# Kernel tuning notes

Measured on AMD Instinct MI355X. Metric: run time of the kernel, lower is better.

The kernel has to match this reference:

```python
import jax, jax.numpy as jnp
import numpy as np

N_NODES = 50000
N_EDGES = 800000
EMBED = 128
HEADS = 8
HEAD_DIM = EMBED // HEADS  # 16
HIDDEN = 512
EPS = 1e-5
SLOPE = 0.2  # DGL GATConv default negative_slope


def setup_inputs() -> dict:
    key = jax.random.key(0)
    ks = jax.random.split(key, 16)
    s = 0.05
    return {
        "x": jax.random.normal(ks[0], (N_NODES, EMBED), dtype=jnp.float32),
        "src": jax.random.randint(ks[1], (N_EDGES,), 0, N_NODES),
        "dst": jax.random.randint(ks[2], (N_EDGES,), 0, N_NODES),
        # GATConv params: fc weight stored as [in, out] (i.e. torch weight transposed)
        "W": jax.random.normal(ks[3], (EMBED, HEADS * HEAD_DIM), dtype=jnp.float32) * s,
        "attn_l": jax.random.normal(ks[4], (HEADS, HEAD_DIM), dtype=jnp.float32) * s,
        "attn_r": jax.random.normal(ks[5], (HEADS, HEAD_DIM), dtype=jnp.float32) * s,
        "gat_bias": jnp.zeros((EMBED,), dtype=jnp.float32),
        # BatchNorm1d affine params (training-mode batch stats used in math)
        "gamma1": jnp.ones((EMBED,), dtype=jnp.float32),
        "beta1": jnp.zeros((EMBED,), dtype=jnp.float32),
        "gamma2": jnp.ones((EMBED,), dtype=jnp.float32),
        "beta2": jnp.zeros((EMBED,), dtype=jnp.float32),
        # FFN weights stored as [in, out]
        "W1": jax.random.normal(ks[6], (EMBED, HIDDEN), dtype=jnp.float32) * s,
        "b1": jnp.zeros((HIDDEN,), dtype=jnp.float32),
        "W2": jax.random.normal(ks[7], (HIDDEN, EMBED), dtype=jnp.float32) * s,
        "b2": jnp.zeros((EMBED,), dtype=jnp.float32),
    }


def _batchnorm(y, gamma, beta):
    mu = jnp.mean(y, axis=0)
    var = jnp.var(y, axis=0)  # biased variance, as torch BN uses for normalization
    return gamma * (y - mu) * jax.lax.rsqrt(var + EPS) + beta


def reference(x, src, dst, W, attn_l, attn_r, gat_bias,
              gamma1, beta1, gamma2, beta2, W1, b1, W2, b2):
    N = x.shape[0]
    # ---- GATConv ----
    feat = (x @ W).reshape(N, HEADS, HEAD_DIM)              # [N,H,D]
    el = jnp.sum(feat * attn_l, axis=-1)                    # [N,H]
    er = jnp.sum(feat * attn_r, axis=-1)                    # [N,H]
    e = jax.nn.leaky_relu(el[src] + er[dst], SLOPE)         # [E,H]
    # segment softmax over incoming edges of each dst node
    m = jax.ops.segment_max(e, dst, num_segments=N)         # [N,H] (-inf for empty)
    ex = jnp.exp(e - m[dst])                                # [E,H]
    denom = jax.ops.segment_sum(ex, dst, num_segments=N)    # [N,H]
    a = ex / denom[dst]                                     # [E,H]
    msg = feat[src] * a[:, :, None]                         # [E,H,D]
    rst = jax.ops.segment_sum(msg, dst, num_segments=N)     # [N,H,D]
    rst = rst + gat_bias.reshape(HEADS, HEAD_DIM)
    h = x + rst.reshape(N, EMBED)                           # skip connection
    # ---- FFN block: BN -> skip(MLP) -> BN ----
    h = _batchnorm(h, gamma1, beta1)
    y = jax.nn.relu(h @ W1 + b1) @ W2 + b2
    h = _batchnorm(h + y, gamma2, beta2)
    return h
```

## Files before the change

### kernel.cpp

```cpp
#include <hip/hip_runtime.h>

#define NCH 128
#define NH  8
#define HID 512
#define SLOPE 0.2f
#define BN_EPS 1e-5f
#define LDP 136
#define NPW 4

typedef __attribute__((ext_vector_type(8))) short short8;
typedef __attribute__((ext_vector_type(4))) float floatx4;

__device__ inline unsigned short f2bf(float f) {
  unsigned u = __float_as_uint(f);
  u += 0x7fffu + ((u >> 16) & 1u);
  return (unsigned short)(u >> 16);
}
__device__ inline float bflo(unsigned u) { return __uint_as_float(u << 16); }
__device__ inline float bfhi(unsigned u) { return __uint_as_float(u & 0xffff0000u); }

__global__ void prep_all(const float* __restrict__ W, unsigned short* __restrict__ WT,
                         const float* __restrict__ W1, unsigned short* __restrict__ w1f,
                         const float* __restrict__ W2, unsigned short* __restrict__ w2f,
                         float* __restrict__ stats, int* __restrict__ cnt, int N) {
  int b = blockIdx.x, tid = threadIdx.x;
  if (b < 64) {
    int i = b * 256 + tid;
    int n = i >> 7, k = i & 127;
    WT[i] = f2bf(W[k * NCH + n]);
  } else if (b < 320) {
    int i = (b - 64) * 256 + tid;
    int ntile = i >> 11, kk = (i >> 9) & 3, lane = (i >> 3) & 63, j = i & 7;
    int k = kk * 32 + (lane >> 4) * 8 + j;
    int n = ntile * 16 + (lane & 15);
    w1f[i] = f2bf(W1[k * HID + n]);
  } else if (b < 576) {
    int i = (b - 320) * 256 + tid;
    int ch = i >> 14, nt = (i >> 11) & 7, kk = (i >> 9) & 3, lane = (i >> 3) & 63, j = i & 7;
    int k = ch * 128 + kk * 32 + (lane >> 4) * 8 + j;
    int n = nt * 16 + (lane & 15);
    w2f[i] = f2bf(W2[k * NCH + n]);
  } else if (b < 596) {
    int i = (b - 576) * 256 + tid;
    ((float4*)stats)[i] = make_float4(0.f, 0.f, 0.f, 0.f);
  } else {
    int i = (b - 596) * 256 + tid;
    int n4 = (N + 3) >> 2;
    if (i < n4) ((int4*)cnt)[i] = make_int4(0, 0, 0, 0);
  }
}

__global__ __launch_bounds__(256) void feat_hist(const float* __restrict__ x,
                                                 const unsigned short* __restrict__ WT,
                                                 const float* __restrict__ attn_l,
                                                 const float* __restrict__ attn_r,
                                                 unsigned short* __restrict__ featb,
                                                 float* __restrict__ el, float* __restrict__ er,
                                                 int N,
                                                 const int* __restrict__ dst, int* __restrict__ cnt,
                                                 int E, int FB) {
  __shared__ unsigned short rowX[64 * LDP];
  __shared__ unsigned short wt[128 * LDP];
  __shared__ float alr[256];
  if (blockIdx.x >= FB) {
    int i = (blockIdx.x - FB) * 256 + threadIdx.x;
    if (i < E) atomicAdd(&cnt[dst[i]], 1);
    return;
  }
  int tid = threadIdx.x;
  int r0 = blockIdx.x * 64;
  int lane = tid & 63, wid = tid >> 6;
  int quad = lane >> 4, lc = lane & 15;
  int mrow = (wid & 1) * 32;
  int chalf = (wid >> 1) * 64;

  alr[tid] = (tid < 128) ? attn_l[tid] : attn_r[tid - 128];
  {
    int n = tid >> 1, kg = (tid & 1) * 64;
    const uint4* g = (const uint4*)(WT + n * NCH + kg);
    uint4* l = (uint4*)&wt[n * LDP + kg];
    for (int i = 0; i < 8; i++) l[i] = g[i];
  }
  {
    int r = tid >> 2, kg = (tid & 3) * 32;
    int gr = r0 + r;
    unsigned short tmp[32];
    if (gr < N) {
      const float4* gp = (const float4*)(x + (size_t)gr * NCH + kg);
      for (int i = 0; i < 8; i++) {
        float4 v = gp[i];
        tmp[i * 4 + 0] = f2bf(v.x); tmp[i * 4 + 1] = f2bf(v.y);
        tmp[i * 4 + 2] = f2bf(v.z); tmp[i * 4 + 3] = f2bf(v.w);
      }
    } else {
      for (int i = 0; i < 32; i++) tmp[i] = 0;
    }
    uint4* l = (uint4*)&rowX[r * LDP + kg];
    const uint4* s = (const uint4*)tmp;
    for (int i = 0; i < 4; i++) l[i] = s[i];
  }
  __syncthreads();

  floatx4 acc[2][4];
  for (int rt = 0; rt < 2; rt++) for (int tt = 0; tt < 4; tt++) acc[rt][tt] = (floatx4)(0.f);
  for (int kk = 0; kk < 4; kk++) {
    short8 a0 = *(const short8*)&rowX[(mrow + lc) * LDP + kk * 32 + quad * 8];
    short8 a1 = *(const short8*)&rowX[(mrow + 16 + lc) * LDP + kk * 32 + quad * 8];
    for (int tt = 0; tt < 4; tt++) {
      short8 b = *(const short8*)&wt[(chalf + tt * 16 + lc) * LDP + kk * 32 + quad * 8];
      acc[0][tt] = __builtin_amdgcn_mfma_f32_16x16x32_bf16(a0, b, acc[0][tt], 0, 0, 0);
      acc[1][tt] = __builtin_amdgcn_mfma_f32_16x16x32_bf16(a1, b, acc[1][tt], 0, 0, 0);
    }
  }
  __syncthreads();
  for (int rt = 0; rt < 2; rt++)
    for (int tt = 0; tt < 4; tt++)
      for (int r = 0; r < 4; r++)
        rowX[(mrow + rt * 16 + quad * 4 + r) * LDP + chalf + tt * 16 + lc] = f2bf(acc[rt][tt][r]);
  __syncthreads();
  {
    int r = tid >> 2, kg = (tid & 3) * 32;
    int gr = r0 + r;
    if (gr < N) {
      uint4* gp = (uint4*)(featb + (size_t)gr * NCH + kg);
      const uint4* l = (const uint4*)&rowX[r * LDP + kg];
      for (int i = 0; i < 4; i++) gp[i] = l[i];
    }
  }
  for (int p = tid; p < 512; p += 256) {
    int row = p >> 3, h = p & 7;
    int gr = r0 + row;
    if (gr < N) {
      const unsigned* rp = (const unsigned*)&rowX[row * LDP + h * 16];
      float sl = 0.f, sr = 0.f;
      for (int q = 0; q < 8; q++) {
        unsigned u = rp[q];
        float lo = bflo(u), hi = bfhi(u);
        int c = h * 16 + 2 * q;
        sl += lo * alr[c] + hi * alr[c + 1];
        sr += lo * alr[128 + c] + hi * alr[128 + c + 1];
      }
      el[gr * NH + h] = sl;
      er[gr * NH + h] = sr;
    }
  }
}

__global__ void scan_part(const int* __restrict__ cnt, int* __restrict__ off,
                          int* __restrict__ bsum, int N) {
  __shared__ int sh[256];
  int t = threadIdx.x, i = blockIdx.x * 256 + t;
  int v = (i < N) ? cnt[i] : 0;
  sh[t] = v; __syncthreads();
  for (int d = 1; d < 256; d <<= 1) {
    int u = (t >= d) ? sh[t - d] : 0;
    __syncthreads();
    sh[t] += u;
    __syncthreads();
  }
  if (i < N) off[i] = sh[t] - v;
  if (t == 255) bsum[blockIdx.x] = sh[255];
}

__global__ void scan_add2(int* __restrict__ off, const int* __restrict__ bsum,
                          int* __restrict__ cursor, int N, int nb) {
  __shared__ int sh[256];
  int t = threadIdx.x;
  int v = (t < nb) ? bsum[t] : 0;
  sh[t] = v; __syncthreads();
  for (int d = 1; d < 256; d <<= 1) {
    int u = (t >= d) ? sh[t - d] : 0;
    __syncthreads();
    sh[t] += u;
    __syncthreads();
  }
  int pref = (blockIdx.x > 0) ? sh[blockIdx.x - 1] : 0;
  int i = blockIdx.x * 256 + t;
  if (i < N) {
    int w = off[i] + pref;
    off[i] = w;
    cursor[i] = w;
  }
}

__global__ void edge_scatter(const int* __restrict__ src, const int* __restrict__ dst,
                             int* __restrict__ cursor, int* __restrict__ ssrc, int E) {
  int i = blockIdx.x * 256 + threadIdx.x;
  if (i < E) {
    int p = atomicAdd(&cursor[dst[i]], 1);
    ssrc[p] = src[i];
  }
}

__global__ __launch_bounds__(256) void gat_gather6(const int* __restrict__ ssrc,
                                                   const int* __restrict__ off,
                                                   const int* __restrict__ cnt,
                                                   const float* __restrict__ el,
                                                   const float* __restrict__ er,
                                                   const unsigned short* __restrict__ featb,
                                                   const float* __restrict__ x,
                                                   const float* __restrict__ gatb,
                                                   float* __restrict__ hbuf,
                                                   float* __restrict__ stats, int N) {
  __shared__ float ps[4][128], pq[4][128];
  int tid = threadIdx.x;
  int lane = tid & 63, w = tid >> 6;
  int hme = lane >> 3;
  int c0 = 2 * lane;
  float gb0 = gatb[c0], gb1 = gatb[c0 + 1];
  float s0 = 0.f, s1 = 0.f, q0 = 0.f, q1 = 0.f;
  int base = blockIdx.x * (4 * NPW) + w * NPW;
  for (int j = 0; j < NPW; j++) {
    int node = base + j;
    if (node >= N) break;
    node = __builtin_amdgcn_readfirstlane(node);
    float erh = er[node * NH + hme];
    int beg = __builtin_amdgcn_readfirstlane(off[node]);
    int num = __builtin_amdgcn_readfirstlane(cnt[node]);
    const int* sp = ssrc + beg;
    float acc0 = 0.f, acc1 = 0.f, den = 0.f;
    int i = 0;
    for (; i + 8 <= num; i += 8) {
      int n0 = __builtin_amdgcn_readfirstlane(sp[i + 0]);
      int n1 = __builtin_amdgcn_readfirstlane(sp[i + 1]);
      int n2 = __builtin_amdgcn_readfirstlane(sp[i + 2]);
      int n3 = __builtin_amdgcn_readfirstlane(sp[i + 3]);
      int n4 = __builtin_amdgcn_readfirstlane(sp[i + 4]);
      int n5 = __builtin_amdgcn_readfirstlane(sp[i + 5]);
      int n6 = __builtin_amdgcn_readfirstlane(sp[i + 6]);
      int n7 = __builtin_amdgcn_readfirstlane(sp[i + 7]);
      unsigned f0 = ((const unsigned*)(featb + (size_t)n0 * NCH))[lane];
      unsigned f1 = ((const unsigned*)(featb + (size_t)n1 * NCH))[lane];
      unsigned f2 = ((const unsigned*)(featb + (size_t)n2 * NCH))[lane];
      unsigned f3 = ((const unsigned*)(featb + (size_t)n3 * NCH))[lane];
      unsigned f4 = ((const unsigned*)(featb + (size_t)n4 * NCH))[lane];
      unsigned f5 = ((const unsigned*)(featb + (size_t)n5 * NCH))[lane];
      unsigned f6 = ((const unsigned*)(featb + (size_t)n6 * NCH))[lane];
      unsigned f7 = ((const unsigned*)(featb + (size_t)n7 * NCH))[lane];
      float e0 = el[n0 * NH + hme] + erh, e1 = el[n1 * NH + hme] + erh;
      float e2 = el[n2 * NH + hme] + erh, e3 = el[n3 * NH + hme] + erh;
      float e4 = el[n4 * NH + hme] + erh, e5 = el[n5 * NH + hme] + erh;
      float e6 = el[n6 * NH + hme] + erh, e7 = el[n7 * NH + hme] + erh;
      e0 = e0 > 0.f ? e0 : SLOPE * e0;  e1 = e1 > 0.f ? e1 : SLOPE * e1;
      e2 = e2 > 0.f ? e2 : SLOPE * e2;  e3 = e3 > 0.f ? e3 : SLOPE * e3;
      e4 = e4 > 0.f ? e4 : SLOPE * e4;  e5 = e5 > 0.f ? e5 : SLOPE * e5;
      e6 = e6 > 0.f ? e6 : SLOPE * e6;  e7 = e7 > 0.f ? e7 : SLOPE * e7;
      float w0 = __expf(e0), w1 = __expf(e1), w2 = __expf(e2), w3 = __expf(e3);
      float w4 = __expf(e4), w5 = __expf(e5), w6 = __expf(e6), w7 = __expf(e7);
      acc0 += w0 * bflo(f0) + w1 * bflo(f1) + w2 * bflo(f2) + w3 * bflo(f3)
            + w4 * bflo(f4) + w5 * bflo(f5) + w6 * bflo(f6) + w7 * bflo(f7);
      acc1 += w0 * bfhi(f0) + w1 * bfhi(f1) + w2 * bfhi(f2) + w3 * bfhi(f3)
            + w4 * bfhi(f4) + w5 * bfhi(f5) + w6 * bfhi(f6) + w7 * bfhi(f7);
      den  += w0 + w1 + w2 + w3 + w4 + w5 + w6 + w7;
    }
    for (; i + 4 <= num; i += 4) {
      int n0 = __builtin_amdgcn_readfirstlane(sp[i + 0]);
      int n1 = __builtin_amdgcn_readfirstlane(sp[i + 1]);
      int n2 = __builtin_amdgcn_readfirstlane(sp[i + 2]);
      int n3 = __builtin_amdgcn_readfirstlane(sp[i + 3]);
      unsigned f0 = ((const unsigned*)(featb + (size_t)n0 * NCH))[lane];
      unsigned f1 = ((const unsigned*)(featb + (size_t)n1 * NCH))[lane];
      unsigned f2 = ((const unsigned*)(featb + (size_t)n2 * NCH))[lane];
      unsigned f3 = ((const unsigned*)(featb + (size_t)n3 * NCH))[lane];
      float e0 = el[n0 * NH + hme] + erh, e1 = el[n1 * NH + hme] + erh;
      float e2 = el[n2 * NH + hme] + erh, e3 = el[n3 * NH + hme] + erh;
      e0 = e0 > 0.f ? e0 : SLOPE * e0;  e1 = e1 > 0.f ? e1 : SLOPE * e1;
      e2 = e2 > 0.f ? e2 : SLOPE * e2;  e3 = e3 > 0.f ? e3 : SLOPE * e3;
      float w0 = __expf(e0), w1 = __expf(e1), w2 = __expf(e2), w3 = __expf(e3);
      acc0 += w0 * bflo(f0) + w1 * bflo(f1) + w2 * bflo(f2) + w3 * bflo(f3);
      acc1 += w0 * bfhi(f0) + w1 * bfhi(f1) + w2 * bfhi(f2) + w3 * bfhi(f3);
      den  += w0 + w1 + w2 + w3;
    }
    for (; i < num; i++) {
      int s = __builtin_amdgcn_readfirstlane(sp[i]);
      unsigned f = ((const unsigned*)(featb + (size_t)s * NCH))[lane];
      float e = el[s * NH + hme] + erh;
      e = e > 0.f ? e : SLOPE * e;
      float wv = __expf(e);
      acc0 += wv * bflo(f); acc1 += wv * bfhi(f); den += wv;
    }
    float inv = den > 0.f ? 1.f / den : 0.f;
    float2 xv = *(const float2*)(x + (size_t)node * NCH + c0);
    float h0 = xv.x + acc0 * inv + gb0;
    float h1 = xv.y + acc1 * inv + gb1;
    *(float2*)(hbuf + (size_t)node * NCH + c0) = make_float2(h0, h1);
    s0 += h0; s1 += h1; q0 += h0 * h0; q1 += h1 * h1;
  }
  ps[w][c0] = s0; ps[w][c0 + 1] = s1;
  pq[w][c0] = q0; pq[w][c0 + 1] = q1;
  __syncthreads();
  if (tid < 128) {
    float ss = ps[0][tid] + ps[1][tid] + ps[2][tid] + ps[3][tid];
    float qq = pq[0][tid] + pq[1][tid] + pq[2][tid] + pq[3][tid];
    int rep = blockIdx.x & 3;
    atomicAdd(&stats[rep * 2048 + tid * 16], ss);
    atomicAdd(&stats[8192 + rep * 2048 + tid * 16], qq);
  }
}

__global__ __launch_bounds__(512, 4) void ffn_mfma2(const float* __restrict__ hbuf,
                                                    const float* __restrict__ g1, const float* __restrict__ be1,
                                                    const unsigned short* __restrict__ w1f,
                                                    const unsigned short* __restrict__ w2f,
                                                    const float* __restrict__ b1, const float* __restrict__ b2,
                                                    float* __restrict__ t, float* __restrict__ stats, int N) {
  __shared__ unsigned short w1t[16384];
  __shared__ unsigned short w2t[16384];
  __shared__ unsigned short scr[8][512];
  __shared__ float b1L[512];
  __shared__ float psc[128], psh[128], b2L[128], csum[128], csq[128];
  int tid = threadIdx.x;
  int lane = tid & 63, wid = tid >> 6;
  int quad = lane >> 4, lc = lane & 15;
  int r0 = blockIdx.x * 128;

  b1L[tid] = b1[tid];
  if (tid < 128) {
    float s = 0.f, sq = 0.f;
    for (int r = 0; r < 4; r++) {
      s  += stats[r * 2048 + tid * 16];
      sq += stats[8192 + r * 2048 + tid * 16];
    }
    float m = s / (float)N;
    float v = sq / (float)N - m * m;
    float rsv = rsqrtf(v + BN_EPS);
    float scv = g1[tid] * rsv;
    psc[tid] = scv;
    psh[tid] = be1[tid] - scv * m;
    b2L[tid] = b2[tid];
    csum[tid] = 0.f; csq[tid] = 0.f;
  }

  int arow = r0 + wid * 16 + lc;
  float4 av[4][2];
  for (int kk = 0; kk < 4; kk++) {
    if (arow < N) {
      const float4* p = (const float4*)(hbuf + (size_t)arow * NCH + kk * 32 + quad * 8);
      av[kk][0] = p[0]; av[kk][1] = p[1];
    } else {
      av[kk][0] = make_float4(0.f, 0.f, 0.f, 0.f);
      av[kk][1] = make_float4(0.f, 0.f, 0.f, 0.f);
    }
  }
  __syncthreads();

  short8 rowA[4];
  for (int kk = 0; kk < 4; kk++) {
    int c = kk * 32 + quad * 8;
    float4 s0 = *(float4*)&psc[c], s1 = *(float4*)&psc[c + 4];
    float4 h0 = *(float4*)&psh[c], h1 = *(float4*)&psh[c + 4];
    short8 r;
    r[0] = (short)f2bf(av[kk][0].x * s0.x + h0.x);
    r[1] = (short)f2bf(av[kk][0].y * s0.y + h0.y);
    r[2] = (short)f2bf(av[kk][0].z * s0.z + h0.z);
    r[3] = (short)f2bf(av[kk][0].w * s0.w + h0.w);
    r[4] = (short)f2bf(av[kk][1].x * s1.x + h1.x);
    r[5] = (short)f2bf(av[kk][1].y * s1.y + h1.y);
    r[6] = (short)f2bf(av[kk][1].z * s1.z + h1.z);
    r[7] = (short)f2bf(av[kk][1].w * s1.w + h1.w);
    rowA[kk] = r;
  }

  floatx4 acc2[8];
  for (int nt = 0; nt < 8; nt++) acc2[nt] = (floatx4)(0.f);

  for (int ch = 0; ch < 4; ch++) {
    __syncthreads();
    {
      const uint4* g1p = (const uint4*)(w1f + ch * 16384);
      const uint4* g2p = (const uint4*)(w2f + ch * 16384);
      uint4* l1 = (uint4*)w1t;
      uint4* l2 = (uint4*)w2t;
      for (int r = 0; r < 4; r++) {
        l1[tid + r * 512] = g1p[tid + r * 512];
        l2[tid + r * 512] = g2p[tid + r * 512];
      }
    }
    __syncthreads();

    for (int kk = 0; kk < 4; kk++) {
      floatx4 d0 = (floatx4)(0.f), d1 = (floatx4)(0.f);
      int t0 = 2 * kk, t1 = 2 * kk + 1;
      for (int kp = 0; kp < 4; kp++) {
        short8 a0 = *(const short8*)&w1t[(t0 * 4 + kp) * 512 + lane * 8];
        short8 a1 = *(const short8*)&w1t[(t1 * 4 + kp) * 512 + lane * 8];
        d0 = __builtin_amdgcn_mfma_f32_16x16x32_bf16(a0, rowA[kp], d0, 0, 0, 0);
        d1 = __builtin_amdgcn_mfma_f32_16x16x32_bf16(a1, rowA[kp], d1, 0, 0, 0);
      }
      {
        int bi0 = ch * 128 + t0 * 16 + 4 * quad;
        float4 bv0 = *(float4*)&b1L[bi0];
        float4 bv1 = *(float4*)&b1L[bi0 + 16];
        float v0, v1, v2, v3;
        unsigned lo, hi;
        int sidx;
        v0 = fmaxf(d0[0] + bv0.x, 0.f); v1 = fmaxf(d0[1] + bv0.y, 0.f);
        v2 = fmaxf(d0[2] + bv0.z, 0.f); v3 = fmaxf(d0[3] + bv0.w, 0.f);
        lo = (unsigned)f2bf(v0) | ((unsigned)f2bf(v1) << 16);
        hi = (unsigned)f2bf(v2) | ((unsigned)f2bf(v3) << 16);
        sidx = ((quad >> 1) * 16 + lc) * 8 + 4 * (quad & 1);
        *(uint2*)&scr[wid][sidx] = make_uint2(lo, hi);
        v0 = fmaxf(d1[0] + bv1.x, 0.f); v1 = fmaxf(d1[1] + bv1.y, 0.f);
        v2 = fmaxf(d1[2] + bv1.z, 0.f); v3 = fmaxf(d1[3] + bv1.w, 0.f);
        lo = (unsigned)f2bf(v0) | ((unsigned)f2bf(v1) << 16);
        hi = (unsigned)f2bf(v2) | ((unsigned)f2bf(v3) << 16);
        sidx = ((2 + (quad >> 1)) * 16 + lc) * 8 + 4 * (quad & 1);
        *(uint2*)&scr[wid][sidx] = make_uint2(lo, hi);
      }
      short8 a2 = *(const short8*)&scr[wid][lane * 8];
      for (int nt = 0; nt < 8; nt++) {
        short8 bfr = *(const short8*)&w2t[(nt * 4 + kk) * 512 + lane * 8];
        acc2[nt] = __builtin_amdgcn_mfma_f32_16x16x32_bf16(a2, bfr, acc2[nt], 0, 0, 0);
      }
    }
  }

  for (int nt = 0; nt < 8; nt++) {
    int col = nt * 16 + lc;
    float sc = psc[col], sh = psh[col], b2v = b2L[col];
    float s = 0.f, q = 0.f;
    for (int reg = 0; reg < 4; reg++) {
      int grow = r0 + wid * 16 + quad * 4 + reg;
      if (grow < N) {
        float hb = hbuf[(size_t)grow * NCH + col];
        float base = __uint_as_float(((unsigned)f2bf(sc * hb + sh)) << 16);
        float tv = base + acc2[nt][reg] + b2v;
        t[(size_t)grow * NCH + col] = tv;
        s += tv; q += tv * tv;
      }
    }
    s += __shfl_xor(s, 16); s += __shfl_xor(s, 32);
    q += __shfl_xor(q, 16); q += __shfl_xor(q, 32);
    if (quad == 0) { atomicAdd(&csum[col], s); atomicAdd(&csq[col], q); }
  }
  __syncthreads();
  if (tid < 128) {
    atomicAdd(&stats[16384 + tid * 16], csum[tid]);
    atomicAdd(&stats[18432 + tid * 16], csq[tid]);
  }
}

__global__ __launch_bounds__(256) void bn2_apply2(const float* __restrict__ t,
                                                  const float* __restrict__ g, const float* __restrict__ b,
                                                  const float* __restrict__ stats,
                                                  float* __restrict__ out, int N) {
  __shared__ float scs[128], shs[128];
  int tid = threadIdx.x;
  if (tid < 128) {
    float s = stats[16384 + tid * 16], sq = stats[18432 + tid * 16];
    float m = s / (float)N;
    float v = sq / (float)N - m * m;
    float rsv = rsqrtf(v + BN_EPS);
    float gg = g[tid] * rsv;
    scs[tid] = gg;
    shs[tid] = b[tid] - gg * m;
  }
  __syncthreads();
  int i = blockIdx.x * 256 + tid;
  int tot4 = N * 32;
  if (i < tot4) {
    float4 v = ((const float4*)t)[i];
    int c = (i & 31) * 4;
    float4 o;
    o.x = v.x * scs[c + 0] + shs[c + 0];
    o.y = v.y * scs[c + 1] + shs[c + 1];
    o.z = v.z * scs[c + 2] + shs[c + 2];
    o.w = v.w * scs[c + 3] + shs[c + 3];
    ((float4*)out)[i] = o;
  }
}

extern "C" void kernel_launch(void* const* d_in, const int* in_sizes, int n_in,
                              void* d_out, int out_size, void* d_ws, size_t ws_size,
                              hipStream_t stream) {
  const float* x       = (const float*)d_in[0];
  const int*   src     = (const int*)d_in[1];
  const int*   dst     = (const int*)d_in[2];
  const float* W       = (const float*)d_in[3];
  const float* attn_l  = (const float*)d_in[4];
  const float* attn_r  = (const float*)d_in[5];
  const float* gatb    = (const float*)d_in[6];
  const float* gamma1  = (const float*)d_in[7];
  const float* beta1   = (const float*)d_in[8];
  const float* gamma2  = (const float*)d_in[9];
  const float* beta2   = (const float*)d_in[10];
  const float* W1      = (const float*)d_in[11];
  const float* b1      = (const float*)d_in[12];
  const float* W2      = (const float*)d_in[13];
  const float* b2      = (const float*)d_in[14];
  float* out = (float*)d_out;

  const int N = in_sizes[0] / NCH;
  const int E = in_sizes[1];
  const int nb = (N + 255) / 256;
  const int EB = (E + 255) / 256;
  const int FB = (N + 63) / 64;

  float* hbuf  = (float*)d_ws;
  float* t     = hbuf + (size_t)N * NCH;
  float* el    = t + (size_t)N * NCH;
  float* er    = el + (size_t)N * NH;
  float* stats = er + (size_t)N * NH;
  float* mus   = stats + 20480;
  unsigned short* featb = (unsigned short*)(mus + 512);
  unsigned short* WT    = featb + (size_t)N * NCH;
  unsigned short* w1f   = WT + NCH * NCH;
  unsigned short* w2f   = w1f + HID * NCH;
  int* cnt    = (int*)(w2f + HID * NCH);
  int* off    = cnt + N;
  int* cursor = off + N;
  int* bsum   = cursor + N;
  int* ssrc   = bsum + 256;

  const int cb = (((N + 3) / 4) + 255) / 256;
  prep_all<<<596 + cb, 256, 0, stream>>>(W, WT, W1, w1f, W2, w2f, stats, cnt, N);

  feat_hist<<<FB + EB, 256, 0, stream>>>(x, WT, attn_l, attn_r, featb, el, er, N,
                                         dst, cnt, E, FB);

  scan_part<<<nb, 256, 0, stream>>>(cnt, off, bsum, N);
  scan_add2<<<nb, 256, 0, stream>>>(off, bsum, cursor, N, nb);
  edge_scatter<<<EB, 256, 0, stream>>>(src, dst, cursor, ssrc, E);

  gat_gather6<<<(N + 4 * NPW - 1) / (4 * NPW), 256, 0, stream>>>(ssrc, off, cnt, el, er, featb,
                                                                 x, gatb, hbuf, stats, N);

  ffn_mfma2<<<(N + 127) / 128, 512, 0, stream>>>(hbuf, gamma1, beta1,
                                                 w1f, w2f, b1, b2, t, stats, N);

  bn2_apply2<<<(N * 32 + 255) / 256, 256, 0, stream>>>(t, gamma2, beta2, stats, out, N);
}
```

Measured before the change: 317.9 us.

## Recompute el in gather from featb, stash normalized rows, repack stats

Drops the precomputed el array. The gather kernel now recomputes each source node's left attention term from the bf16 feature word it already loads, using the attn_l weights and three xor-shuffle reductions across the 8 lanes of each head. This removes one scattered global load per edge and the el writes, at the cost of extra ALU and shuffle work per edge. Separately, the FFN epilogue reuses the bf16 normalized rows stashed in LDS instead of re-reading hbuf and recomputing BN1, and the BN1 stats are reorganised into 8 dense replicas instead of 4 strided ones.

```diff
diff --git a/kernel.cpp b/kernel.cpp
--- a/kernel.cpp
+++ b/kernel.cpp
@@ -52,16 +52,15 @@
 
 __global__ __launch_bounds__(256) void feat_hist(const float* __restrict__ x,
                                                  const unsigned short* __restrict__ WT,
-                                                 const float* __restrict__ attn_l,
                                                  const float* __restrict__ attn_r,
                                                  unsigned short* __restrict__ featb,
-                                                 float* __restrict__ el, float* __restrict__ er,
+                                                 float* __restrict__ er,
                                                  int N,
                                                  const int* __restrict__ dst, int* __restrict__ cnt,
                                                  int E, int FB) {
   __shared__ unsigned short rowX[64 * LDP];
   __shared__ unsigned short wt[128 * LDP];
-  __shared__ float alr[256];
+  __shared__ float arL[128];
   if (blockIdx.x >= FB) {
     int i = (blockIdx.x - FB) * 256 + threadIdx.x;
     if (i < E) atomicAdd(&cnt[dst[i]], 1);
@@ -74,7 +73,7 @@
   int mrow = (wid & 1) * 32;
   int chalf = (wid >> 1) * 64;
 
-  alr[tid] = (tid < 128) ? attn_l[tid] : attn_r[tid - 128];
+  if (tid < 128) arL[tid] = attn_r[tid];
   {
     int n = tid >> 1, kg = (tid & 1) * 64;
     const uint4* g = (const uint4*)(WT + n * NCH + kg);
@@ -132,15 +131,12 @@
     int gr = r0 + row;
     if (gr < N) {
       const unsigned* rp = (const unsigned*)&rowX[row * LDP + h * 16];
-      float sl = 0.f, sr = 0.f;
+      float sr = 0.f;
       for (int q = 0; q < 8; q++) {
         unsigned u = rp[q];
-        float lo = bflo(u), hi = bfhi(u);
         int c = h * 16 + 2 * q;
-        sl += lo * alr[c] + hi * alr[c + 1];
-        sr += lo * alr[128 + c] + hi * alr[128 + c + 1];
-      }
-      el[gr * NH + h] = sl;
+        sr += bflo(u) * arL[c] + bfhi(u) * arL[c + 1];
+      }
       er[gr * NH + h] = sr;
     }
   }
@@ -192,10 +188,10 @@
   }
 }
 
-__global__ __launch_bounds__(256) void gat_gather6(const int* __restrict__ ssrc,
+__global__ __launch_bounds__(256) void gat_gather7(const int* __restrict__ ssrc,
                                                    const int* __restrict__ off,
                                                    const int* __restrict__ cnt,
-                                                   const float* __restrict__ el,
+                                                   const float* __restrict__ attn_l,
                                                    const float* __restrict__ er,
                                                    const unsigned short* __restrict__ featb,
                                                    const float* __restrict__ x,
@@ -207,6 +203,8 @@
   int lane = tid & 63, w = tid >> 6;
   int hme = lane >> 3;
   int c0 = 2 * lane;
+  float2 al2 = *(const float2*)(attn_l + c0);
+  float alx = al2.x, aly = al2.y;
   float gb0 = gatb[c0], gb1 = gatb[c0 + 1];
   float s0 = 0.f, s1 = 0.f, q0 = 0.f, q1 = 0.f;
   int base = blockIdx.x * (4 * NPW) + w * NPW;
@@ -237,10 +235,28 @@
       unsigned f5 = ((const unsigned*)(featb + (size_t)n5 * NCH))[lane];
       unsigned f6 = ((const unsigned*)(featb + (size_t)n6 * NCH))[lane];
       unsigned f7 = ((const unsigned*)(featb + (size_t)n7 * NCH))[lane];
-      float e0 = el[n0 * NH + hme] + erh, e1 = el[n1 * NH + hme] + erh;
-      float e2 = el[n2 * NH + hme] + erh, e3 = el[n3 * NH + hme] + erh;
-      float e4 = el[n4 * NH + hme] + erh, e5 = el[n5 * NH + hme] + erh;
-      float e6 = el[n6 * NH + hme] + erh, e7 = el[n7 * NH + hme] + erh;
+      float p0 = bflo(f0) * alx + bfhi(f0) * aly;
+      float p1 = bflo(f1) * alx + bfhi(f1) * aly;
+      float p2 = bflo(f2) * alx + bfhi(f2) * aly;
+      float p3 = bflo(f3) * alx + bfhi(f3) * aly;
+      float p4 = bflo(f4) * alx + bfhi(f4) * aly;
+      float p5 = bflo(f5) * alx + bfhi(f5) * aly;
+      float p6 = bflo(f6) * alx + bfhi(f6) * aly;
+      float p7 = bflo(f7) * alx + bfhi(f7) * aly;
+      p0 += __shfl_xor(p0, 1); p1 += __shfl_xor(p1, 1);
+      p2 += __shfl_xor(p2, 1); p3 += __shfl_xor(p3, 1);
+      p4 += __shfl_xor(p4, 1); p5 += __shfl_xor(p5, 1);
+      p6 += __shfl_xor(p6, 1); p7 += __shfl_xor(p7, 1);
+      p0 += __shfl_xor(p0, 2); p1 += __shfl_xor(p1, 2);
+      p2 += __shfl_xor(p2, 2); p3 += __shfl_xor(p3, 2);
+      p4 += __shfl_xor(p4, 2); p5 += __shfl_xor(p5, 2);
+      p6 += __shfl_xor(p6, 2); p7 += __shfl_xor(p7, 2);
+      p0 += __shfl_xor(p0, 4); p1 += __shfl_xor(p1, 4);
+      p2 += __shfl_xor(p2, 4); p3 += __shfl_xor(p3, 4);
+      p4 += __shfl_xor(p4, 4); p5 += __shfl_xor(p5, 4);
+      p6 += __shfl_xor(p6, 4); p7 += __shfl_xor(p7, 4);
+      float e0 = p0 + erh, e1 = p1 + erh, e2 = p2 + erh, e3 = p3 + erh;
+      float e4 = p4 + erh, e5 = p5 + erh, e6 = p6 + erh, e7 = p7 + erh;
       e0 = e0 > 0.f ? e0 : SLOPE * e0;  e1 = e1 > 0.f ? e1 : SLOPE * e1;
       e2 = e2 > 0.f ? e2 : SLOPE * e2;  e3 = e3 > 0.f ? e3 : SLOPE * e3;
       e4 = e4 > 0.f ? e4 : SLOPE * e4;  e5 = e5 > 0.f ? e5 : SLOPE * e5;
@@ -253,28 +269,12 @@
             + w4 * bfhi(f4) + w5 * bfhi(f5) + w6 * bfhi(f6) + w7 * bfhi(f7);
       den  += w0 + w1 + w2 + w3 + w4 + w5 + w6 + w7;
     }
-    for (; i + 4 <= num; i += 4) {
-      int n0 = __builtin_amdgcn_readfirstlane(sp[i + 0]);
-      int n1 = __builtin_amdgcn_readfirstlane(sp[i + 1]);
-      int n2 = __builtin_amdgcn_readfirstlane(sp[i + 2]);
-      int n3 = __builtin_amdgcn_readfirstlane(sp[i + 3]);
-      unsigned f0 = ((const unsigned*)(featb + (size_t)n0 * NCH))[lane];
-      unsigned f1 = ((const unsigned*)(featb + (size_t)n1 * NCH))[lane];
-      unsigned f2 = ((const unsigned*)(featb + (size_t)n2 * NCH))[lane];
-      unsigned f3 = ((const unsigned*)(featb + (size_t)n3 * NCH))[lane];
-      float e0 = el[n0 * NH + hme] + erh, e1 = el[n1 * NH + hme] + erh;
-      float e2 = el[n2 * NH + hme] + erh, e3 = el[n3 * NH + hme] + erh;
-      e0 = e0 > 0.f ? e0 : SLOPE * e0;  e1 = e1 > 0.f ? e1 : SLOPE * e1;
-      e2 = e2 > 0.f ? e2 : SLOPE * e2;  e3 = e3 > 0.f ? e3 : SLOPE * e3;
-      float w0 = __expf(e0), w1 = __expf(e1), w2 = __expf(e2), w3 = __expf(e3);
-      acc0 += w0 * bflo(f0) + w1 * bflo(f1) + w2 * bflo(f2) + w3 * bflo(f3);
-      acc1 += w0 * bfhi(f0) + w1 * bfhi(f1) + w2 * bfhi(f2) + w3 * bfhi(f3);
-      den  += w0 + w1 + w2 + w3;
-    }
     for (; i < num; i++) {
       int s = __builtin_amdgcn_readfirstlane(sp[i]);
       unsigned f = ((const unsigned*)(featb + (size_t)s * NCH))[lane];
-      float e = el[s * NH + hme] + erh;
+      float p = bflo(f) * alx + bfhi(f) * aly;
+      p += __shfl_xor(p, 1); p += __shfl_xor(p, 2); p += __shfl_xor(p, 4);
+      float e = p + erh;
       e = e > 0.f ? e : SLOPE * e;
       float wv = __expf(e);
       acc0 += wv * bflo(f); acc1 += wv * bfhi(f); den += wv;
@@ -292,9 +292,9 @@
   if (tid < 128) {
     float ss = ps[0][tid] + ps[1][tid] + ps[2][tid] + ps[3][tid];
     float qq = pq[0][tid] + pq[1][tid] + pq[2][tid] + pq[3][tid];
-    int rep = blockIdx.x & 3;
-    atomicAdd(&stats[rep * 2048 + tid * 16], ss);
-    atomicAdd(&stats[8192 + rep * 2048 + tid * 16], qq);
+    int rep = blockIdx.x & 7;
+    atomicAdd(&stats[rep * 128 + tid], ss);
+    atomicAdd(&stats[1024 + rep * 128 + tid], qq);
   }
 }
 
@@ -317,9 +317,9 @@
   b1L[tid] = b1[tid];
   if (tid < 128) {
     float s = 0.f, sq = 0.f;
-    for (int r = 0; r < 4; r++) {
-      s  += stats[r * 2048 + tid * 16];
-      sq += stats[8192 + r * 2048 + tid * 16];
+    for (int r = 0; r < 8; r++) {
+      s  += stats[r * 128 + tid];
+      sq += stats[1024 + r * 128 + tid];
     }
     float m = s / (float)N;
     float v = sq / (float)N - m * m;
@@ -415,15 +415,22 @@
     }
   }
 
+  __syncthreads();
+  {
+    unsigned short* stash = w1t;
+    for (int kk = 0; kk < 4; kk++)
+      *(short8*)&stash[wid * 2048 + lc * 128 + kk * 32 + quad * 8] = rowA[kk];
+  }
+  __syncthreads();
+
   for (int nt = 0; nt < 8; nt++) {
     int col = nt * 16 + lc;
-    float sc = psc[col], sh = psh[col], b2v = b2L[col];
+    float b2v = b2L[col];
     float s = 0.f, q = 0.f;
     for (int reg = 0; reg < 4; reg++) {
       int grow = r0 + wid * 16 + quad * 4 + reg;
       if (grow < N) {
-        float hb = hbuf[(size_t)grow * NCH + col];
-        float base = __uint_as_float(((unsigned)f2bf(sc * hb + sh)) << 16);
+        float base = bflo((unsigned)w1t[wid * 2048 + (quad * 4 + reg) * 128 + col]);
         float tv = base + acc2[nt][reg] + b2v;
         t[(size_t)grow * NCH + col] = tv;
         s += tv; q += tv * tv;
@@ -498,11 +505,9 @@
 
   float* hbuf  = (float*)d_ws;
   float* t     = hbuf + (size_t)N * NCH;
-  float* el    = t + (size_t)N * NCH;
-  float* er    = el + (size_t)N * NH;
+  float* er    = t + (size_t)N * NCH;
   float* stats = er + (size_t)N * NH;
-  float* mus   = stats + 20480;
-  unsigned short* featb = (unsigned short*)(mus + 512);
+  unsigned short* featb = (unsigned short*)(stats + 20480);
   unsigned short* WT    = featb + (size_t)N * NCH;
   unsigned short* w1f   = WT + NCH * NCH;
   unsigned short* w2f   = w1f + HID * NCH;
@@ -515,15 +520,14 @@
   const int cb = (((N + 3) / 4) + 255) / 256;
   prep_all<<<596 + cb, 256, 0, stream>>>(W, WT, W1, w1f, W2, w2f, stats, cnt, N);
 
-  feat_hist<<<FB + EB, 256, 0, stream>>>(x, WT, attn_l, attn_r, featb, el, er, N,
-                                         dst, cnt, E, FB);
+  feat_hist<<<FB + EB, 256, 0, stream>>>(x, WT, attn_r, featb, er, N, dst, cnt, E, FB);
 
   scan_part<<<nb, 256, 0, stream>>>(cnt, off, bsum, N);
   scan_add2<<<nb, 256, 0, stream>>>(off, bsum, cursor, N, nb);
   edge_scatter<<<EB, 256, 0, stream>>>(src, dst, cursor, ssrc, E);
 
-  gat_gather6<<<(N + 4 * NPW - 1) / (4 * NPW), 256, 0, stream>>>(ssrc, off, cnt, el, er, featb,
-                                                                 x, gatb, hbuf, stats, N);
+  gat_gather7<<<(N + 4 * NPW - 1) / (4 * NPW), 256, 0, stream>>>(ssrc, off, cnt, attn_l, er,
+                                                                 featb, x, gatb, hbuf, stats, N);
 
   ffn_mfma2<<<(N + 127) / 128, 512, 0, stream>>>(hbuf, gamma1, beta1,
                                                  w1f, w2f, b1, b2, t, stats, N);
```

Measured after the change: 296.9 us. 6.6% less time.
